# Kernel optimization log

Hardware: AMD Instinct MI355X
Metric: run time of the kernel (lower is better)

Reference implementation:

```python
import jax, jax.numpy as jnp
import numpy as np

T = 0.2          # temperature
W = 0.1          # loss weight
BIG = 2 ** 30    # sentinel label for masked-out samples


def setup_inputs() -> dict:
    key = jax.random.key(0)
    k1, k2, k3, k4 = jax.random.split(key, 4)
    bs, C, Gn, S = 32, 128, 256, 16
    grouped_features = jax.random.normal(k1, (bs, C, Gn, S), dtype=jnp.float32)
    # instance labels in [-1, 8): -1 = background
    proposal_instance_mask = jax.random.randint(k2, (bs, Gn, S), -1, 8, dtype=jnp.int32)
    # seed indices with duplicates possible (range 40 over 16 samples)
    grouped_indices = jax.random.randint(k3, (bs, Gn, S), 0, 40, dtype=jnp.int32)
    context_compen = jax.random.normal(k4, (1, C), dtype=jnp.float32)
    return {
        "proposal_instance_mask": proposal_instance_mask,
        "grouped_features": grouped_features,
        "grouped_indices": grouped_indices,
        "context_compen": context_compen,
    }


def _group_loss(feat, idx, lab, ctx):
    # feat: [S, C], idx: [S], lab: [S], ctx: [C]
    # NOTE: sum_{a,b} f_a . g_b / (n_f * n_g) == mean(f) . mean(g), so the
    # original tiny-mm contrastive loss reduces to pairwise dots of per-instance means.
    S, C = feat.shape
    pos = jnp.arange(S)
    # unique count of seed indices -> truncate to first u samples (as in torch code)
    si = jnp.sort(idx)
    u = 1 + jnp.sum(si[1:] != si[:-1])
    valid = pos < u
    lab_m = jnp.where(valid, lab, BIG)
    # per-group unique labels (sorted), jit-friendly
    sl = jnp.sort(lab_m)
    new = jnp.concatenate([jnp.ones((1,), bool), sl[1:] != sl[:-1]])
    cid = jnp.cumsum(new) - 1                      # compact id of each sorted label
    uniq = jnp.full((S,), BIG, sl.dtype).at[cid].set(sl)
    n_labels = jnp.sum(new & (sl != BIG))          # number of distinct valid labels
    has_bg = uniq[0] == -1                         # -1 sorts first if present
    # per-instance mean features via segment scatter-add
    comp = jnp.searchsorted(uniq, lab_m)           # sample -> compact instance slot
    sums = jnp.zeros((S, C), feat.dtype).at[comp].add(jnp.where(valid[:, None], feat, 0.0))
    cnts = jnp.zeros((S,), feat.dtype).at[comp].add(valid.astype(feat.dtype))
    means = sums / jnp.maximum(cnts, 1.0)[:, None]
    hb = has_bg.astype(jnp.int32)
    fg_count = n_labels - hb
    inst_num = fg_count + 1                        # bg slot always present
    # row 0 = bg mean (or context_compen if no bg), rows 1.. = fg means
    gidx = jnp.clip(pos + hb - 1, 0, S - 1)
    M = means[gidx]
    M = M.at[0].set(jnp.where(has_bg, M[0], ctx))
    inst_valid = pos < inst_num
    sim = (M @ M.T) / T                            # [S, S] tiny matmul of means
    sim_m = jnp.where(inst_valid[None, :], sim, -jnp.inf)
    lse = jax.scipy.special.logsumexp(sim_m, axis=1)
    li = lse - jnp.diagonal(sim)                   # -log(pos/(pos+neg)) per fg row
    fg_mask = inst_valid & (pos >= 1)
    gl = jnp.sum(jnp.where(fg_mask, li, 0.0)) / jnp.maximum(inst_num - 1, 1).astype(feat.dtype)
    return gl, fg_count >= 1


def reference(proposal_instance_mask, grouped_features, grouped_indices, context_compen):
    bs, C, Gn, S = grouped_features.shape
    feats = grouped_features.transpose(0, 2, 3, 1).reshape(-1, S, C)  # [G, S, C]
    idxs = grouped_indices.reshape(-1, S)
    labs = proposal_instance_mask.reshape(-1, S)
    ctx = context_compen[0]
    gl, gv = jax.vmap(lambda f, i, l: _group_loss(f, i, l, ctx))(feats, idxs, labs)
    gvf = gv.astype(gl.dtype)
    return jnp.sum(gl * gvf) / jnp.sum(gvf) * W
```

## Files before the change

kernel.cpp:

```cpp
#include <hip/hip_runtime.h>

#define GQ   8192
#define WPB  2

#define LDS_FENCE() asm volatile("s_waitcnt lgkmcnt(0)" ::: "memory")

template <int CTRL>
__device__ __forceinline__ float dpp_add(float x) {
    int t = __builtin_amdgcn_update_dpp(0, __float_as_int(x), CTRL, 0xf, 0xf, true);
    return x + __int_as_float(t);
}
__device__ __forceinline__ float wave_sum64(float x) {
    x = dpp_add<0x111>(x);
    x = dpp_add<0x112>(x);
    x = dpp_add<0x114>(x);
    x = dpp_add<0x118>(x);
    x = dpp_add<0x142>(x);
    x = dpp_add<0x143>(x);
    return x;
}
__device__ __forceinline__ float row_sum16(float x) {
    x = dpp_add<0x111>(x);
    x = dpp_add<0x112>(x);
    x = dpp_add<0x114>(x);
    x = dpp_add<0x118>(x);
    return x;
}
__device__ __forceinline__ float rdlane_f(float x, int lane) {
    return __int_as_float(__builtin_amdgcn_readlane(__float_as_int(x), lane));
}

__global__ __launch_bounds__(64 * WPB, 4) void group_loss_kernel(
    const int*   __restrict__ labs,
    const float* __restrict__ feats,
    const int*   __restrict__ idxs,
    const float* __restrict__ ctx,
    float2* __restrict__ ws)
{
    __shared__ float SH[WPB * 48];

    const int l  = threadIdx.x & 63;
    const int wu = threadIdx.x >> 6;
    float* SIMM = SH + wu * 48;

    const int blk = blockIdx.x;
    const int g  = ((blk & 7) << 10) | ((blk >> 3) << 1) | wu;
    const int b  = g >> 8;
    const int gn = g & 255;
    const long fbase = (long)b * (128 * 256 * 16) + (long)gn * 16;

    const float* gp0 = feats + fbase + (long)l * 4096;
    const float* gp1 = gp0 + 64 * 4096;
    float4 A[4], B[4];
    #pragma unroll
    for (int q = 0; q < 4; ++q) A[q] = *(const float4*)(gp0 + q * 4);
    #pragma unroll
    for (int q = 0; q < 4; ++q) B[q] = *(const float4*)(gp1 + q * 4);
    const float cx0 = ctx[l], cx1 = ctx[l + 64];
    float fa[16], fb[16];
    #pragma unroll
    for (int q = 0; q < 4; ++q) {
        fa[4*q+0] = A[q].x; fa[4*q+1] = A[q].y; fa[4*q+2] = A[q].z; fa[4*q+3] = A[q].w;
        fb[4*q+0] = B[q].x; fb[4*q+1] = B[q].y; fb[4*q+2] = B[q].z; fb[4*q+3] = B[q].w;
    }

    int myidx = -1, mylab = -2;
    if (l < 16) { myidx = idxs[g * 16 + l]; mylab = labs[g * 16 + l]; }

    unsigned long long dupm = 0ULL;
    #pragma unroll
    for (int j = 0; j < 15; ++j) {
        const int sj = __builtin_amdgcn_readlane(myidx, j);
        const unsigned long long eq = __ballot(myidx == sj);
        dupm |= (eq & ~((2ULL << j) - 1ULL));
    }
    const int u = __popcll(~dupm & 0xFFFFULL);

    const bool valid = l < u;
    const int bid = valid ? (mylab + 1) : 255;

    int cnt[9];
    #pragma unroll
    for (int r = 0; r < 9; ++r) cnt[r] = __popcll(__ballot(bid == r));
    const bool has_bg = cnt[0] > 0;
    int fg_count = 0, pm = 0;
    #pragma unroll
    for (int r = 1; r < 9; ++r)
        if (cnt[r] > 0) { ++fg_count; pm |= 1 << r; }

    float m0[9] = {0,0,0,0,0,0,0,0,0};
    float m1[9] = {0,0,0,0,0,0,0,0,0};
    #pragma unroll
    for (int s = 0; s < 16; ++s) {
        if (s < u) {
            const int bs = __builtin_amdgcn_readlane(bid, s);
            switch (bs) {
                case 0: m0[0] += fa[s]; m1[0] += fb[s]; break;
                case 1: m0[1] += fa[s]; m1[1] += fb[s]; break;
                case 2: m0[2] += fa[s]; m1[2] += fb[s]; break;
                case 3: m0[3] += fa[s]; m1[3] += fb[s]; break;
                case 4: m0[4] += fa[s]; m1[4] += fb[s]; break;
                case 5: m0[5] += fa[s]; m1[5] += fb[s]; break;
                case 6: m0[6] += fa[s]; m1[6] += fb[s]; break;
                case 7: m0[7] += fa[s]; m1[7] += fb[s]; break;
                case 8: m0[8] += fa[s]; m1[8] += fb[s]; break;
            }
        }
    }
    #pragma unroll
    for (int r = 0; r < 9; ++r) {
        const float invc = 1.0f / (float)(cnt[r] > 0 ? cnt[r] : 1);
        m0[r] *= invc; m1[r] *= invc;
    }
    if (!has_bg) { m0[0] = cx0; m1[0] = cx1; }

    float mine = 0.0f;
    {
        int p = 0;
        #pragma unroll
        for (int i = 1; i <= 8; ++i) {
            #pragma unroll
            for (int j = 0; j <= i; ++j) {
                float x = m0[i] * m0[j] + m1[i] * m1[j];
                x = wave_sum64(x);
                const float sv = rdlane_f(x, 63);
                mine = (l == p) ? sv : mine;
                ++p;
            }
        }
    }
    mine *= 5.0f;

    if (l < 44) SIMM[l] = mine;
    LDS_FENCE();

    float li_val = 0.0f;
    if (l >= 1 && l < 9 && ((pm >> l) & 1)) {
        const int r = l;
        float srow[9];
        #pragma unroll
        for (int j = 0; j < 9; ++j) {
            const int ii = (r > j) ? r : j;
            const int jj = (r > j) ? j : r;
            srow[j] = SIMM[ii * (ii + 1) / 2 - 1 + jj];
        }
        float vmax = srow[0];
        #pragma unroll
        for (int j = 1; j < 9; ++j)
            if ((pm >> j) & 1) vmax = fmaxf(vmax, srow[j]);
        float se = __expf(srow[0] - vmax);
        #pragma unroll
        for (int j = 1; j < 9; ++j)
            if ((pm >> j) & 1) se += __expf(srow[j] - vmax);
        li_val = vmax + __logf(se) - srow[r];
    }

    const float ssum = row_sum16(li_val);
    const float tot  = rdlane_f(ssum, 15);
    if (l == 0) {
        float2 r;
        r.x = tot / (float)(fg_count > 0 ? fg_count : 1);
        r.y = (fg_count > 0) ? 1.0f : 0.0f;
        ws[g] = r;
    }
}

__global__ __launch_bounds__(1024) void reduce_kernel(
    const float2* __restrict__ ws, float* __restrict__ out)
{
    __shared__ float sa[1024], sb[1024];
    const int t = threadIdx.x;
    float a = 0.0f, b2 = 0.0f;
    for (int g = t; g < GQ; g += 1024) {
        float2 v = ws[g];
        a += v.x; b2 += v.y;
    }
    sa[t] = a; sb[t] = b2;
    __syncthreads();
    for (int off = 512; off > 0; off >>= 1) {
        if (t < off) { sa[t] += sa[t + off]; sb[t] += sb[t + off]; }
        __syncthreads();
    }
    if (t == 0) out[0] = 0.1f * (sa[0] / sb[0]);
}

extern "C" void kernel_launch(void* const* d_in, const int* in_sizes, int n_in,
                              void* d_out, int out_size, void* d_ws, size_t ws_size,
                              hipStream_t stream) {
    const int*   labs  = (const int*)d_in[0];
    const float* feats = (const float*)d_in[1];
    const int*   idxs  = (const int*)d_in[2];
    const float* ctx   = (const float*)d_in[3];
    float* out = (float*)d_out;
    float2* ws = (float2*)d_ws;

    group_loss_kernel<<<GQ / WPB, 64 * WPB, 0, stream>>>(labs, feats, idxs, ctx, ws);
    reduce_kernel<<<1, 1024, 0, stream>>>(ws, out);
}
```

Baseline: 115.2 us.

## Process four groups per wave with double-buffered feature prefetch

Each wave now loops over four consecutive groups and prefetches the next group's features, indices and labels into a second register buffer while computing the current one. Blocks grow to four waves and the grid shrinks accordingly. The reduce kernel reads float4 pairs. The aim is to hide global load latency inside a wave, at the cost of fewer resident waves and higher register pressure. The explicit LDS wait fence is also removed.

```diff
diff --git a/kernel.cpp b/kernel.cpp
--- a/kernel.cpp
+++ b/kernel.cpp
@@ -1,9 +1,9 @@
 #include <hip/hip_runtime.h>
 
-#define GQ   8192
-#define WPB  2
-
-#define LDS_FENCE() asm volatile("s_waitcnt lgkmcnt(0)" ::: "memory")
+#define GQ    8192
+#define WPB   4
+#define GPW   4
+#define NBLK  (GQ / (WPB * GPW))
 
 template <int CTRL>
 __device__ __forceinline__ float dpp_add(float x) {
@@ -29,8 +29,9 @@
 __device__ __forceinline__ float rdlane_f(float x, int lane) {
     return __int_as_float(__builtin_amdgcn_readlane(__float_as_int(x), lane));
 }
-
-__global__ __launch_bounds__(64 * WPB, 4) void group_loss_kernel(
+#define COMP(v4, k) ((k)==0?(v4).x:((k)==1?(v4).y:((k)==2?(v4).z:(v4).w)))
+
+__global__ __launch_bounds__(64 * WPB, 2) void group_loss_kernel(
     const int*   __restrict__ labs,
     const float* __restrict__ feats,
     const int*   __restrict__ idxs,
@@ -44,136 +45,153 @@
     float* SIMM = SH + wu * 48;
 
     const int blk = blockIdx.x;
-    const int g  = ((blk & 7) << 10) | ((blk >> 3) << 1) | wu;
-    const int b  = g >> 8;
-    const int gn = g & 255;
-    const long fbase = (long)b * (128 * 256 * 16) + (long)gn * 16;
-
-    const float* gp0 = feats + fbase + (long)l * 4096;
-    const float* gp1 = gp0 + 64 * 4096;
-    float4 A[4], B[4];
-    #pragma unroll
-    for (int q = 0; q < 4; ++q) A[q] = *(const float4*)(gp0 + q * 4);
-    #pragma unroll
-    for (int q = 0; q < 4; ++q) B[q] = *(const float4*)(gp1 + q * 4);
+    const int gbase = ((blk & 7) << 10) | ((blk >> 3) << 4) | (wu << 2);
+    const int b  = gbase >> 8;
+    const int gn = gbase & 255;
+    const long fb0 = (long)b * (128 * 256 * 16) + (long)gn * 16;
+    const float* gp = feats + fb0 + (long)l * 4096;
+
     const float cx0 = ctx[l], cx1 = ctx[l + 64];
-    float fa[16], fb[16];
+
+    float4 buf[2][8];
+    int blab[2] = {-2, -2}, bidx[2] = {-1, -1};
     #pragma unroll
     for (int q = 0; q < 4; ++q) {
-        fa[4*q+0] = A[q].x; fa[4*q+1] = A[q].y; fa[4*q+2] = A[q].z; fa[4*q+3] = A[q].w;
-        fb[4*q+0] = B[q].x; fb[4*q+1] = B[q].y; fb[4*q+2] = B[q].z; fb[4*q+3] = B[q].w;
-    }
-
-    int myidx = -1, mylab = -2;
-    if (l < 16) { myidx = idxs[g * 16 + l]; mylab = labs[g * 16 + l]; }
-
-    unsigned long long dupm = 0ULL;
+        buf[0][q]     = *(const float4*)(gp + q * 4);
+        buf[0][4 + q] = *(const float4*)(gp + 64 * 4096 + q * 4);
+    }
+    if (l < 16) { bidx[0] = idxs[gbase * 16 + l]; blab[0] = labs[gbase * 16 + l]; }
+
     #pragma unroll
-    for (int j = 0; j < 15; ++j) {
-        const int sj = __builtin_amdgcn_readlane(myidx, j);
-        const unsigned long long eq = __ballot(myidx == sj);
-        dupm |= (eq & ~((2ULL << j) - 1ULL));
-    }
-    const int u = __popcll(~dupm & 0xFFFFULL);
-
-    const bool valid = l < u;
-    const int bid = valid ? (mylab + 1) : 255;
-
-    int cnt[9];
-    #pragma unroll
-    for (int r = 0; r < 9; ++r) cnt[r] = __popcll(__ballot(bid == r));
-    const bool has_bg = cnt[0] > 0;
-    int fg_count = 0, pm = 0;
-    #pragma unroll
-    for (int r = 1; r < 9; ++r)
-        if (cnt[r] > 0) { ++fg_count; pm |= 1 << r; }
-
-    float m0[9] = {0,0,0,0,0,0,0,0,0};
-    float m1[9] = {0,0,0,0,0,0,0,0,0};
-    #pragma unroll
-    for (int s = 0; s < 16; ++s) {
-        if (s < u) {
-            const int bs = __builtin_amdgcn_readlane(bid, s);
-            switch (bs) {
-                case 0: m0[0] += fa[s]; m1[0] += fb[s]; break;
-                case 1: m0[1] += fa[s]; m1[1] += fb[s]; break;
-                case 2: m0[2] += fa[s]; m1[2] += fb[s]; break;
-                case 3: m0[3] += fa[s]; m1[3] += fb[s]; break;
-                case 4: m0[4] += fa[s]; m1[4] += fb[s]; break;
-                case 5: m0[5] += fa[s]; m1[5] += fb[s]; break;
-                case 6: m0[6] += fa[s]; m1[6] += fb[s]; break;
-                case 7: m0[7] += fa[s]; m1[7] += fb[s]; break;
-                case 8: m0[8] += fa[s]; m1[8] += fb[s]; break;
-            }
-        }
-    }
-    #pragma unroll
-    for (int r = 0; r < 9; ++r) {
-        const float invc = 1.0f / (float)(cnt[r] > 0 ? cnt[r] : 1);
-        m0[r] *= invc; m1[r] *= invc;
-    }
-    if (!has_bg) { m0[0] = cx0; m1[0] = cx1; }
-
-    float mine = 0.0f;
-    {
-        int p = 0;
-        #pragma unroll
-        for (int i = 1; i <= 8; ++i) {
-            #pragma unroll
-            for (int j = 0; j <= i; ++j) {
-                float x = m0[i] * m0[j] + m1[i] * m1[j];
-                x = wave_sum64(x);
-                const float sv = rdlane_f(x, 63);
-                mine = (l == p) ? sv : mine;
-                ++p;
-            }
-        }
-    }
-    mine *= 5.0f;
-
-    if (l < 44) SIMM[l] = mine;
-    LDS_FENCE();
-
-    float li_val = 0.0f;
-    if (l >= 1 && l < 9 && ((pm >> l) & 1)) {
-        const int r = l;
-        float srow[9];
-        #pragma unroll
-        for (int j = 0; j < 9; ++j) {
-            const int ii = (r > j) ? r : j;
-            const int jj = (r > j) ? j : r;
-            srow[j] = SIMM[ii * (ii + 1) / 2 - 1 + jj];
-        }
-        float vmax = srow[0];
-        #pragma unroll
-        for (int j = 1; j < 9; ++j)
-            if ((pm >> j) & 1) vmax = fmaxf(vmax, srow[j]);
-        float se = __expf(srow[0] - vmax);
-        #pragma unroll
-        for (int j = 1; j < 9; ++j)
-            if ((pm >> j) & 1) se += __expf(srow[j] - vmax);
-        li_val = vmax + __logf(se) - srow[r];
-    }
-
-    const float ssum = row_sum16(li_val);
-    const float tot  = rdlane_f(ssum, 15);
-    if (l == 0) {
-        float2 r;
-        r.x = tot / (float)(fg_count > 0 ? fg_count : 1);
-        r.y = (fg_count > 0) ? 1.0f : 0.0f;
-        ws[g] = r;
+    for (int t = 0; t < GPW; ++t) {
+        const int cur = t & 1, nxt = cur ^ 1;
+
+        if (t + 1 < GPW) {
+            const float* gq = gp + 16 * (t + 1);
+            #pragma unroll
+            for (int q = 0; q < 4; ++q) {
+                buf[nxt][q]     = *(const float4*)(gq + q * 4);
+                buf[nxt][4 + q] = *(const float4*)(gq + 64 * 4096 + q * 4);
+            }
+            if (l < 16) {
+                bidx[nxt] = idxs[(gbase + t + 1) * 16 + l];
+                blab[nxt] = labs[(gbase + t + 1) * 16 + l];
+            }
+        }
+
+        const int g = gbase + t;
+        const int myidx = (l < 16) ? bidx[cur] : -1;
+        const int mylab = (l < 16) ? blab[cur] : -2;
+
+        unsigned long long dupm = 0ULL;
+        #pragma unroll
+        for (int j = 0; j < 15; ++j) {
+            const int sj = __builtin_amdgcn_readlane(myidx, j);
+            const unsigned long long eq = __ballot(myidx == sj);
+            dupm |= (eq & ~((2ULL << j) - 1ULL));
+        }
+        const int u = __popcll(~dupm & 0xFFFFULL);
+
+        const bool valid = l < u;
+        const int bid = valid ? (mylab + 1) : 255;
+
+        int cnt[9];
+        #pragma unroll
+        for (int r = 0; r < 9; ++r) cnt[r] = __popcll(__ballot(bid == r));
+        const bool has_bg = cnt[0] > 0;
+        int fg_count = 0, pm = 0;
+        #pragma unroll
+        for (int r = 1; r < 9; ++r)
+            if (cnt[r] > 0) { ++fg_count; pm |= 1 << r; }
+
+        float m0[9] = {0,0,0,0,0,0,0,0,0};
+        float m1[9] = {0,0,0,0,0,0,0,0,0};
+        #pragma unroll
+        for (int s = 0; s < 16; ++s) {
+            if (s < u) {
+                const int bs = __builtin_amdgcn_readlane(bid, s);
+                const float fas = COMP(buf[cur][s >> 2], s & 3);
+                const float fbs = COMP(buf[cur][4 + (s >> 2)], s & 3);
+                switch (bs) {
+                    case 0: m0[0] += fas; m1[0] += fbs; break;
+                    case 1: m0[1] += fas; m1[1] += fbs; break;
+                    case 2: m0[2] += fas; m1[2] += fbs; break;
+                    case 3: m0[3] += fas; m1[3] += fbs; break;
+                    case 4: m0[4] += fas; m1[4] += fbs; break;
+                    case 5: m0[5] += fas; m1[5] += fbs; break;
+                    case 6: m0[6] += fas; m1[6] += fbs; break;
+                    case 7: m0[7] += fas; m1[7] += fbs; break;
+                    case 8: m0[8] += fas; m1[8] += fbs; break;
+                }
+            }
+        }
+        #pragma unroll
+        for (int r = 0; r < 9; ++r) {
+            const float invc = 1.0f / (float)(cnt[r] > 0 ? cnt[r] : 1);
+            m0[r] *= invc; m1[r] *= invc;
+        }
+        if (!has_bg) { m0[0] = cx0; m1[0] = cx1; }
+
+        float mine = 0.0f;
+        {
+            int p = 0;
+            #pragma unroll
+            for (int i = 1; i <= 8; ++i) {
+                #pragma unroll
+                for (int j = 0; j <= i; ++j) {
+                    float x = m0[i] * m0[j] + m1[i] * m1[j];
+                    x = wave_sum64(x);
+                    const float sv = rdlane_f(x, 63);
+                    mine = (l == p) ? sv : mine;
+                    ++p;
+                }
+            }
+        }
+        mine *= 5.0f;
+
+        if (l < 44) SIMM[l] = mine;
+
+        float li_val = 0.0f;
+        if (l >= 1 && l < 9 && ((pm >> l) & 1)) {
+            const int r = l;
+            float srow[9];
+            #pragma unroll
+            for (int j = 0; j < 9; ++j) {
+                const int ii = (r > j) ? r : j;
+                const int jj = (r > j) ? j : r;
+                srow[j] = SIMM[ii * (ii + 1) / 2 - 1 + jj];
+            }
+            float vmax = srow[0];
+            #pragma unroll
+            for (int j = 1; j < 9; ++j)
+                if ((pm >> j) & 1) vmax = fmaxf(vmax, srow[j]);
+            float se = __expf(srow[0] - vmax);
+            #pragma unroll
+            for (int j = 1; j < 9; ++j)
+                if ((pm >> j) & 1) se += __expf(srow[j] - vmax);
+            li_val = vmax + __logf(se) - srow[r];
+        }
+
+        const float ssum = row_sum16(li_val);
+        const float tot  = rdlane_f(ssum, 15);
+        if (l == 0) {
+            float2 r;
+            r.x = tot / (float)(fg_count > 0 ? fg_count : 1);
+            r.y = (fg_count > 0) ? 1.0f : 0.0f;
+            ws[g] = r;
+        }
     }
 }
 
 __global__ __launch_bounds__(1024) void reduce_kernel(
-    const float2* __restrict__ ws, float* __restrict__ out)
+    const float4* __restrict__ ws4, float* __restrict__ out)
 {
     __shared__ float sa[1024], sb[1024];
     const int t = threadIdx.x;
     float a = 0.0f, b2 = 0.0f;
-    for (int g = t; g < GQ; g += 1024) {
-        float2 v = ws[g];
-        a += v.x; b2 += v.y;
+    for (int i = t; i < GQ / 2; i += 1024) {
+        float4 v = ws4[i];
+        a += v.x + v.z; b2 += v.y + v.w;
     }
     sa[t] = a; sb[t] = b2;
     __syncthreads();
@@ -194,6 +212,6 @@
     float* out = (float*)d_out;
     float2* ws = (float2*)d_ws;
 
-    group_loss_kernel<<<GQ / WPB, 64 * WPB, 0, stream>>>(labs, feats, idxs, ctx, ws);
-    reduce_kernel<<<1, 1024, 0, stream>>>(ws, out);
-}
+    group_loss_kernel<<<NBLK, 64 * WPB, 0, stream>>>(labs, feats, idxs, ctx, ws);
+    reduce_kernel<<<1, 1024, 0, stream>>>((const float4*)ws, out);
+}
```

Result: slower. 130.5 us (+13.3%).
